# Optimization experiments

Measured on AMD Instinct MI355X. Metric: run time of the kernel, lower is better.

Reference implementation:

```python
import jax, jax.numpy as jnp
from jax import lax
import numpy as np

BATCH, SEQ, VOCAB, EMB, UNIT = 256, 512, 50000, 128, 512


def setup_inputs() -> dict:
    key = jax.random.key(0)
    ks = jax.random.split(key, 8)
    s = 0.05  # keep tanh out of saturation
    return {
        "tokens": jax.random.randint(ks[0], (BATCH, SEQ), 0, VOCAB, dtype=jnp.int32),
        "emb": jax.random.normal(ks[1], (VOCAB, EMB), jnp.float32) * s,
        "Wx0": jax.random.normal(ks[2], (EMB, UNIT), jnp.float32) * s,
        "Wh0": jax.random.normal(ks[3], (UNIT, UNIT), jnp.float32) * s,
        "b0": jnp.zeros((UNIT,), jnp.float32),
        "Wx1": jax.random.normal(ks[4], (UNIT, UNIT), jnp.float32) * s,
        "Wh1": jax.random.normal(ks[5], (UNIT, UNIT), jnp.float32) * s,
        "b1": jnp.zeros((UNIT,), jnp.float32),
        "fc_w": jax.random.normal(ks[6], (UNIT, 1), jnp.float32) * s,
        "fc_b": jnp.zeros((1,), jnp.float32),
    }


def reference(tokens, emb, Wx0, Wh0, b0, Wx1, Wh1, b1, fc_w, fc_b):
    # Embedding lookup: [B, T, E]
    x = emb[tokens]
    B = tokens.shape[0]
    U = Wh0.shape[0]

    def step(carry, xt):
        h0, h1, h2 = carry
        # SimpleRNNCell: h' = tanh(x @ Wx + h @ Wh + b); dropout inactive (training=None)
        h0n = jnp.tanh(xt @ Wx0 + h0 @ Wh0 + b0)
        # NOTE: original code reuses rnncell1 weights for both layer 1 and layer 2 (bug kept)
        h1n = jnp.tanh(h0n @ Wx1 + h1 @ Wh1 + b1)
        h2n = jnp.tanh(h1n @ Wx1 + h2 @ Wh1 + b1)
        return (h0n, h1n, h2n), None

    init = tuple(jnp.zeros((B, U), x.dtype) for _ in range(3))
    (h0, h1, h2), _ = lax.scan(step, init, jnp.swapaxes(x, 0, 1))  # scan over time [T, B, E]
    logits = h2 @ fc_w + fc_b  # [B, 1]
    return jax.nn.sigmoid(logits)
```

## Files before the change

kernel.cpp:

```cpp
#include <hip/hip_runtime.h>


#define BATCH 256
#define SEQ   512
#define EMBD  128
#define UNIT  512

typedef _Float16 half8 __attribute__((ext_vector_type(8)));
typedef _Float16 half4 __attribute__((ext_vector_type(4)));
typedef float    f32x4 __attribute__((ext_vector_type(4)));
typedef unsigned int uint4v __attribute__((ext_vector_type(4)));
typedef int      int4v __attribute__((ext_vector_type(4)));

#define FLAGS_BYTES 4096
#define HBUF_OFF    4096
#define HBUF_ELEMS  (3*8*4*32*512)
#define HBUF_BYTES  (HBUF_ELEMS*2)
#define PWX0_OFF    (HBUF_OFF + HBUF_BYTES)
#define PWH0_OFF    (PWX0_OFF + EMBD*UNIT*2)
#define PWX1_OFF    (PWH0_OFF + UNIT*UNIT*2)
#define PWH1_OFF    (PWX1_OFF + UNIT*UNIT*2)

__device__ __forceinline__ void sc_st_int(int* p, int v) {
    asm volatile("global_store_dword %0, %1, off sc0 sc1" :: "v"(p), "v"(v) : "memory");
}

__device__ __forceinline__ void sc_ld_q3(const int* p0, const int* p1, const int* p2,
                                         int4v& a, int4v& b, int4v& c) {
    asm volatile(
        "global_load_dwordx4 %0, %3, off sc0 sc1\n\t"
        "global_load_dwordx4 %1, %4, off sc0 sc1\n\t"
        "global_load_dwordx4 %2, %5, off sc0 sc1\n\t"
        "s_waitcnt vmcnt(0)"
        : "=&v"(a), "=&v"(b), "=&v"(c)
        : "v"(p0), "v"(p1), "v"(p2)
        : "memory");
}

__device__ __forceinline__ void sc_load14(
    const uint4v* a0, const uint4v* a1, const uint4v* a2,
    const uint4v* a3, const uint4v* a4, const uint4v* a5,
    const uint4v* b0, const uint4v* b1, const uint4v* b2, const uint4v* b3,
    const uint4v* b4, const uint4v* b5, const uint4v* b6, const uint4v* b7,
    uint4v& s0, uint4v& s1, uint4v& s2, uint4v& s3, uint4v& s4, uint4v& s5,
    uint4v& r0, uint4v& r1, uint4v& r2, uint4v& r3,
    uint4v& r4, uint4v& r5, uint4v& r6, uint4v& r7)
{
    asm volatile(
        "global_load_dwordx4 %0, %14, off sc0 sc1\n\t"
        "global_load_dwordx4 %1, %15, off sc0 sc1\n\t"
        "global_load_dwordx4 %2, %16, off sc0 sc1\n\t"
        "global_load_dwordx4 %3, %17, off sc0 sc1\n\t"
        "global_load_dwordx4 %4, %18, off sc0 sc1\n\t"
        "global_load_dwordx4 %5, %19, off sc0 sc1\n\t"
        "global_load_dwordx4 %6, %20, off sc0 sc1\n\t"
        "global_load_dwordx4 %7, %21, off sc0 sc1\n\t"
        "global_load_dwordx4 %8, %22, off sc0 sc1\n\t"
        "global_load_dwordx4 %9, %23, off sc0 sc1\n\t"
        "global_load_dwordx4 %10, %24, off sc0 sc1\n\t"
        "global_load_dwordx4 %11, %25, off sc0 sc1\n\t"
        "global_load_dwordx4 %12, %26, off sc0 sc1\n\t"
        "global_load_dwordx4 %13, %27, off sc0 sc1\n\t"
        "s_waitcnt vmcnt(0)"
        : "=&v"(s0), "=&v"(s1), "=&v"(s2), "=&v"(s3), "=&v"(s4), "=&v"(s5),
          "=&v"(r0), "=&v"(r1), "=&v"(r2), "=&v"(r3),
          "=&v"(r4), "=&v"(r5), "=&v"(r6), "=&v"(r7)
        : "v"(a0), "v"(a1), "v"(a2), "v"(a3), "v"(a4), "v"(a5),
          "v"(b0), "v"(b1), "v"(b2), "v"(b3), "v"(b4), "v"(b5), "v"(b6), "v"(b7)
        : "memory");
}

__device__ __forceinline__ void sc_load6(
    const uint4v* p0, const uint4v* p1, const uint4v* p2,
    const uint4v* p3, const uint4v* p4, const uint4v* p5,
    uint4v& r0, uint4v& r1, uint4v& r2, uint4v& r3, uint4v& r4, uint4v& r5)
{
    asm volatile(
        "global_load_dwordx4 %0, %6, off sc0 sc1\n\t"
        "global_load_dwordx4 %1, %7, off sc0 sc1\n\t"
        "global_load_dwordx4 %2, %8, off sc0 sc1\n\t"
        "global_load_dwordx4 %3, %9, off sc0 sc1\n\t"
        "global_load_dwordx4 %4, %10, off sc0 sc1\n\t"
        "global_load_dwordx4 %5, %11, off sc0 sc1\n\t"
        "s_waitcnt vmcnt(0)"
        : "=&v"(r0), "=&v"(r1), "=&v"(r2), "=&v"(r3), "=&v"(r4), "=&v"(r5)
        : "v"(p0), "v"(p1), "v"(p2), "v"(p3), "v"(p4), "v"(p5)
        : "memory");
}

__device__ __forceinline__ void sc_store2(uint4v* p0, uint4v v0, uint4v* p1, uint4v v1) {
    asm volatile(
        "global_store_dwordx4 %0, %2, off sc0 sc1\n\t"
        "global_store_dwordx4 %1, %3, off sc0 sc1\n\t"
        "s_waitcnt vmcnt(0)"
        :: "v"(p0), "v"(p1), "v"(v0), "v"(v1)
        : "memory");
}

__global__ void zero_ws_kernel(uint4v* __restrict__ p, int n16) {
    int i = blockIdx.x * 256 + threadIdx.x;
    uint4v z = {0u, 0u, 0u, 0u};
    if (i < n16) p[i] = z;
}

__global__ void pack_w_kernel(const float* __restrict__ src, _Float16* __restrict__ dst,
                              int K, int N) {
    int idx = blockIdx.x * 256 + threadIdx.x;
    if (idx >= K * N) return;
    int j    = idx & 7;
    int lane = (idx >> 3) & 63;
    int rest = idx >> 9;
    int KT   = K >> 5;
    int kt   = rest % KT;
    int nt   = rest / KT;
    int k = kt*32 + (lane >> 4)*8 + j;
    int n = nt*16 + (lane & 15);
    dst[idx] = (_Float16)src[k * N + n];
}

__global__ __launch_bounds__(256, 1)
void rnn_main_kernel(const int*   __restrict__ tokens,
                     const float* __restrict__ emb,
                     const float* __restrict__ b0,
                     const float* __restrict__ b1,
                     char* ws)
{
    const int bid   = blockIdx.x;
    const int layer = bid >> 5;
    const int mg    = (bid >> 2) & 7;
    const int ns    = bid & 3;
    const int tid   = threadIdx.x;
    const int wv    = tid >> 6;
    const int lane  = tid & 63;
    const int q     = lane >> 4;
    const int c16   = lane & 15;

    int* flags = (int*)ws;
    int* qOwn  = flags + (layer*8 + mg)*32;
    int* qUp   = flags + ((layer > 0 ? layer-1 : layer)*8 + mg)*32;
    int* qDn   = flags + ((layer < 2 ? layer+1 : layer)*8 + mg)*32;

    _Float16* hbuf = (_Float16*)(ws + HBUF_OFF);
    const _Float16* pWh = (const _Float16*)(ws + (layer == 0 ? PWH0_OFF : PWH1_OFF));
    const _Float16* pWx = (const _Float16*)(ws + (layer == 0 ? PWX0_OFF : PWX1_OFF));
    const float* bias = (layer == 0) ? b0 : b1;

    const int c0  = ns*128 + wv*32;
    const int nt0 = c0 >> 4;

    __shared__ _Float16 Ah [32][512];
    __shared__ _Float16 Ain[32][512];
    __shared__ _Float16 Bounce[32][128];

    {
        uint4v z = {0u,0u,0u,0u};
#pragma unroll
        for (int i = 0; i < 8; ++i) ((uint4v*)Ah)[i*256 + tid] = z;
    }

    half8 whf[16][2];
    half8 wxf[16][2];
#pragma unroll
    for (int kt = 0; kt < 16; ++kt)
#pragma unroll
        for (int n = 0; n < 2; ++n)
            whf[kt][n] = *(const half8*)&pWh[(((nt0 + n)*16 + kt)*64 + lane) * 8];
    if (layer == 0) {
#pragma unroll
        for (int kt = 0; kt < 4; ++kt)
#pragma unroll
            for (int n = 0; n < 2; ++n)
                wxf[kt][n] = *(const half8*)&pWx[(((nt0 + n)*4 + kt)*64 + lane) * 8];
    } else {
#pragma unroll
        for (int kt = 0; kt < 16; ++kt)
#pragma unroll
            for (int n = 0; n < 2; ++n)
                wxf[kt][n] = *(const half8*)&pWx[(((nt0 + n)*16 + kt)*64 + lane) * 8];
    }

    const float bv0 = bias[c0 + c16];
    const float bv1 = bias[c0 + 16 + c16];

    const int m0       = mg * 32;
    const int slotBase = (layer*8 + mg) * 4;

    const int sA = (ns == 0) ? 1 : 0;
    const int sB = (ns <= 1) ? 2 : 1;
    const int sC = (ns <= 2) ? 3 : 2;

    for (int t = 0; t < SEQ; ++t) {
        if (tid == 0) {
            for (;;) {
                int4v o, u, d;
                sc_ld_q3(qOwn, qUp, qDn, o, u, d);
                int mo = o[0] < o[1] ? o[0] : o[1];
                mo = mo < o[2] ? mo : o[2]; mo = mo < o[3] ? mo : o[3];
                int mu = u[0] < u[1] ? u[0] : u[1];
                mu = mu < u[2] ? mu : u[2]; mu = mu < u[3] ? mu : u[3];
                int md = d[0] < d[1] ? d[0] : d[1];
                md = md < d[2] ? md : d[2]; md = md < d[3] ? md : d[3];
                bool ok = (mo >= t);
                if (layer > 0)            ok = ok && (mu >= t + 1);
                if (layer < 2 && t >= 4)  ok = ok && (md >= t - 3);
                if (ok) break;
                __builtin_amdgcn_s_sleep(1);
            }
        }
        __syncthreads();

        const uint4v* tp = (const uint4v*)(hbuf + (slotBase + ((t + 3) & 3)) * 16384);
        const int j0 = 2*tid, j1 = j0 + 1;
        const int r0i = j0 >> 4, cl0 = j0 & 15;
        const int r1i = j1 >> 4, cl1 = j1 & 15;
        const int ccA0 = sA*16 + cl0, ccA1 = sA*16 + cl1;
        const int ccB0 = sB*16 + cl0, ccB1 = sB*16 + cl1;
        const int ccC0 = sC*16 + cl0, ccC1 = sC*16 + cl1;

        f32x4 acc00 = {0,0,0,0}, acc01 = {0,0,0,0}, acc10 = {0,0,0,0}, acc11 = {0,0,0,0};

        if (layer > 0) {
            const uint4v* sb = (const uint4v*)
                (hbuf + (((layer-1)*8 + mg)*4 + (t & 3)) * 16384);
            uint4v s0,s1,s2,s3,s4,s5, rr0,rr1,rr2,rr3,rr4,rr5,rr6,rr7;
            sc_load14(tp + r0i*64 + ccA0, tp + r1i*64 + ccA1,
                      tp + r0i*64 + ccB0, tp + r1i*64 + ccB1,
                      tp + r0i*64 + ccC0, tp + r1i*64 + ccC1,
                      sb +        tid, sb +  256 + tid, sb +  512 + tid, sb +  768 + tid,
                      sb + 1024 + tid, sb + 1280 + tid, sb + 1536 + tid, sb + 1792 + tid,
                      s0, s1, s2, s3, s4, s5,
                      rr0, rr1, rr2, rr3, rr4, rr5, rr6, rr7);
            *(uint4v*)&Ah[r0i][((ccA0 + r0i) & 63) * 8] = s0;
            *(uint4v*)&Ah[r1i][((ccA1 + r1i) & 63) * 8] = s1;
            *(uint4v*)&Ah[r0i][((ccB0 + r0i) & 63) * 8] = s2;
            *(uint4v*)&Ah[r1i][((ccB1 + r1i) & 63) * 8] = s3;
            *(uint4v*)&Ah[r0i][((ccC0 + r0i) & 63) * 8] = s4;
            *(uint4v*)&Ah[r1i][((ccC1 + r1i) & 63) * 8] = s5;
#pragma unroll
            for (int i = 0; i < 8; ++i) {
                uint4v v = (i==0)?rr0:(i==1)?rr1:(i==2)?rr2:(i==3)?rr3:
                           (i==4)?rr4:(i==5)?rr5:(i==6)?rr6:rr7;
                int ci = i*256 + tid;
                int r  = ci >> 6;
                int cc = ci & 63;
                *(uint4v*)&Ain[r][((cc + r) & 63) * 8] = v;
            }
            __syncthreads();

#pragma unroll
            for (int kt = 0; kt < 16; ++kt) {
                half8 a0 = *(const half8*)&Ah[c16]     [((kt*4 + q + c16)      & 63) * 8];
                half8 a1 = *(const half8*)&Ah[16 + c16][((kt*4 + q + 16 + c16) & 63) * 8];
                acc00 = __builtin_amdgcn_mfma_f32_16x16x32_f16(a0, whf[kt][0], acc00, 0, 0, 0);
                acc01 = __builtin_amdgcn_mfma_f32_16x16x32_f16(a0, whf[kt][1], acc01, 0, 0, 0);
                acc10 = __builtin_amdgcn_mfma_f32_16x16x32_f16(a1, whf[kt][0], acc10, 0, 0, 0);
                acc11 = __builtin_amdgcn_mfma_f32_16x16x32_f16(a1, whf[kt][1], acc11, 0, 0, 0);
            }
#pragma unroll
            for (int kt = 0; kt < 16; ++kt) {
                half8 a0 = *(const half8*)&Ain[c16]     [((kt*4 + q + c16)      & 63) * 8];
                half8 a1 = *(const half8*)&Ain[16 + c16][((kt*4 + q + 16 + c16) & 63) * 8];
                acc00 = __builtin_amdgcn_mfma_f32_16x16x32_f16(a0, wxf[kt][0], acc00, 0, 0, 0);
                acc01 = __builtin_amdgcn_mfma_f32_16x16x32_f16(a0, wxf[kt][1], acc01, 0, 0, 0);
                acc10 = __builtin_amdgcn_mfma_f32_16x16x32_f16(a1, wxf[kt][0], acc10, 0, 0, 0);
                acc11 = __builtin_amdgcn_mfma_f32_16x16x32_f16(a1, wxf[kt][1], acc11, 0, 0, 0);
            }
        } else {
            uint4v s0, s1, s2, s3, s4, s5;
            sc_load6(tp + r0i*64 + ccA0, tp + r1i*64 + ccA1,
                     tp + r0i*64 + ccB0, tp + r1i*64 + ccB1,
                     tp + r0i*64 + ccC0, tp + r1i*64 + ccC1,
                     s0, s1, s2, s3, s4, s5);
            *(uint4v*)&Ah[r0i][((ccA0 + r0i) & 63) * 8] = s0;
            *(uint4v*)&Ah[r1i][((ccA1 + r1i) & 63) * 8] = s1;
            *(uint4v*)&Ah[r0i][((ccB0 + r0i) & 63) * 8] = s2;
            *(uint4v*)&Ah[r1i][((ccB1 + r1i) & 63) * 8] = s3;
            *(uint4v*)&Ah[r0i][((ccC0 + r0i) & 63) * 8] = s4;
            *(uint4v*)&Ah[r1i][((ccC1 + r1i) & 63) * 8] = s5;
#pragma unroll
            for (int i = 0; i < 4; ++i) {
                int idx = i*256 + tid;
                int r   = idx >> 5;
                int qq  = idx & 31;
                int tok = tokens[(m0 + r)*SEQ + t];
                float4 f = *((const float4*)(emb + (long)tok * EMBD) + qq);
                half4 h = { (_Float16)f.x, (_Float16)f.y, (_Float16)f.z, (_Float16)f.w };
                *(half4*)&Ain[r][((((qq >> 1) + r) & 63) * 8) + (qq & 1) * 4] = h;
            }
            __syncthreads();

#pragma unroll
            for (int kt = 0; kt < 16; ++kt) {
                half8 a0 = *(const half8*)&Ah[c16]     [((kt*4 + q + c16)      & 63) * 8];
                half8 a1 = *(const half8*)&Ah[16 + c16][((kt*4 + q + 16 + c16) & 63) * 8];
                acc00 = __builtin_amdgcn_mfma_f32_16x16x32_f16(a0, whf[kt][0], acc00, 0, 0, 0);
                acc01 = __builtin_amdgcn_mfma_f32_16x16x32_f16(a0, whf[kt][1], acc01, 0, 0, 0);
                acc10 = __builtin_amdgcn_mfma_f32_16x16x32_f16(a1, whf[kt][0], acc10, 0, 0, 0);
                acc11 = __builtin_amdgcn_mfma_f32_16x16x32_f16(a1, whf[kt][1], acc11, 0, 0, 0);
            }
#pragma unroll
            for (int kt = 0; kt < 4; ++kt) {
                half8 a0 = *(const half8*)&Ain[c16]     [((kt*4 + q + c16)      & 63) * 8];
                half8 a1 = *(const half8*)&Ain[16 + c16][((kt*4 + q + 16 + c16) & 63) * 8];
                acc00 = __builtin_amdgcn_mfma_f32_16x16x32_f16(a0, wxf[kt][0], acc00, 0, 0, 0);
                acc01 = __builtin_amdgcn_mfma_f32_16x16x32_f16(a0, wxf[kt][1], acc01, 0, 0, 0);
                acc10 = __builtin_amdgcn_mfma_f32_16x16x32_f16(a1, wxf[kt][0], acc10, 0, 0, 0);
                acc11 = __builtin_amdgcn_mfma_f32_16x16x32_f16(a1, wxf[kt][1], acc11, 0, 0, 0);
            }
        }

        _Float16 hv[16];
#pragma unroll
        for (int r = 0; r < 4; ++r) {
            int row0 = q*4 + r, row1 = 16 + row0;
            float z, e; _Float16 v;
            z = acc00[r] + bv0; e = __expf(2.0f*z); v = (_Float16)(1.0f - 2.0f/(e + 1.0f));
            hv[r*4+0] = v; Bounce[row0][wv*32 + c16]      = v;
            z = acc01[r] + bv1; e = __expf(2.0f*z); v = (_Float16)(1.0f - 2.0f/(e + 1.0f));
            hv[r*4+1] = v; Bounce[row0][wv*32 + 16 + c16] = v;
            z = acc10[r] + bv0; e = __expf(2.0f*z); v = (_Float16)(1.0f - 2.0f/(e + 1.0f));
            hv[r*4+2] = v; Bounce[row1][wv*32 + c16]      = v;
            z = acc11[r] + bv1; e = __expf(2.0f*z); v = (_Float16)(1.0f - 2.0f/(e + 1.0f));
            hv[r*4+3] = v; Bounce[row1][wv*32 + 16 + c16] = v;
        }
        __syncthreads();

        {
            int g0 = c0 + c16, g1 = c0 + 16 + c16;
#pragma unroll
            for (int r = 0; r < 4; ++r) {
                int row0 = q*4 + r, row1 = 16 + row0;
                Ah[row0][(((g0 >> 3) + row0) & 63)*8 + (g0 & 7)] = hv[r*4+0];
                Ah[row0][(((g1 >> 3) + row0) & 63)*8 + (g1 & 7)] = hv[r*4+1];
                Ah[row1][(((g0 >> 3) + row1) & 63)*8 + (g0 & 7)] = hv[r*4+2];
                Ah[row1][(((g1 >> 3) + row1) & 63)*8 + (g1 & 7)] = hv[r*4+3];
            }
            _Float16* tc = hbuf + (slotBase + (t & 3)) * 16384;
            uint4v v0 = ((const uint4v*)Bounce)[j0];
            uint4v v1 = ((const uint4v*)Bounce)[j1];
            uint4v* d0 = (uint4v*)(tc + (j0 >> 4)*512 + ns*128) + (j0 & 15);
            uint4v* d1 = (uint4v*)(tc + (j1 >> 4)*512 + ns*128) + (j1 & 15);
            sc_store2(d0, v0, d1, v1);
        }
        __syncthreads();
        if (tid == 0) sc_st_int(qOwn + ns, t + 1);
    }
}

__global__ void fc_kernel(const char* __restrict__ ws,
                          const float* __restrict__ fc_w,
                          const float* __restrict__ fc_b,
                          float* __restrict__ out)
{
    int row  = blockIdx.x;
    int lane = threadIdx.x;
    int m = row >> 5, lr = row & 31;
    const _Float16* h2 = (const _Float16*)(ws + HBUF_OFF)
                         + (((2*8 + m)*4 + 3) * 16384)
                         + lr * UNIT;
    half8 hv = *(const half8*)&h2[lane * 8];
    const float* w = fc_w + lane * 8;
    float s = 0.0f;
#pragma unroll
    for (int j = 0; j < 8; ++j) s += (float)hv[j] * w[j];
#pragma unroll
    for (int off = 32; off > 0; off >>= 1) s += __shfl_down(s, off);
    if (lane == 0) {
        float logit = s + fc_b[0];
        out[row] = 1.0f / (1.0f + __expf(-logit));
    }
}

extern "C" void kernel_launch(void* const* d_in, const int* in_sizes, int n_in,
                              void* d_out, int out_size, void* d_ws, size_t ws_size,
                              hipStream_t stream)
{
    const int*   tokens = (const int*)  d_in[0];
    const float* emb    = (const float*)d_in[1];
    const float* Wx0    = (const float*)d_in[2];
    const float* Wh0    = (const float*)d_in[3];
    const float* b0     = (const float*)d_in[4];
    const float* Wx1    = (const float*)d_in[5];
    const float* Wh1    = (const float*)d_in[6];
    const float* b1     = (const float*)d_in[7];
    const float* fcw    = (const float*)d_in[8];
    const float* fcb    = (const float*)d_in[9];
    char*  ws  = (char*)d_ws;
    float* out = (float*)d_out;

    int n16 = (FLAGS_BYTES + HBUF_BYTES) / 16;
    zero_ws_kernel<<<(n16 + 255)/256, 256, 0, stream>>>((uint4v*)ws, n16);

    pack_w_kernel<<<(EMBD*UNIT + 255)/256, 256, 0, stream>>>(Wx0, (_Float16*)(ws + PWX0_OFF), EMBD, UNIT);
    pack_w_kernel<<<(UNIT*UNIT + 255)/256, 256, 0, stream>>>(Wh0, (_Float16*)(ws + PWH0_OFF), UNIT, UNIT);
    pack_w_kernel<<<(UNIT*UNIT + 255)/256, 256, 0, stream>>>(Wx1, (_Float16*)(ws + PWX1_OFF), UNIT, UNIT);
    pack_w_kernel<<<(UNIT*UNIT + 255)/256, 256, 0, stream>>>(Wh1, (_Float16*)(ws + PWH1_OFF), UNIT, UNIT);

    rnn_main_kernel<<<96, 256, 0, stream>>>(tokens, emb, b0, b1, ws);

    fc_kernel<<<256, 64, 0, stream>>>((const char*)ws, fcw, fcb, out);
}
```

Baseline: 2.636 ms.

## Remap blocks so each batch group shares an XCD and use XCD-scope coherence

```diff
diff --git a/kernel.cpp b/kernel.cpp
--- a/kernel.cpp
+++ b/kernel.cpp
@@ -44,57 +44,104 @@
     const uint4v* b4, const uint4v* b5, const uint4v* b6, const uint4v* b7,
     uint4v& s0, uint4v& s1, uint4v& s2, uint4v& s3, uint4v& s4, uint4v& s5,
     uint4v& r0, uint4v& r1, uint4v& r2, uint4v& r3,
-    uint4v& r4, uint4v& r5, uint4v& r6, uint4v& r7)
+    uint4v& r4, uint4v& r5, uint4v& r6, uint4v& r7, bool fast)
 {
-    asm volatile(
-        "global_load_dwordx4 %0, %14, off sc0 sc1\n\t"
-        "global_load_dwordx4 %1, %15, off sc0 sc1\n\t"
-        "global_load_dwordx4 %2, %16, off sc0 sc1\n\t"
-        "global_load_dwordx4 %3, %17, off sc0 sc1\n\t"
-        "global_load_dwordx4 %4, %18, off sc0 sc1\n\t"
-        "global_load_dwordx4 %5, %19, off sc0 sc1\n\t"
-        "global_load_dwordx4 %6, %20, off sc0 sc1\n\t"
-        "global_load_dwordx4 %7, %21, off sc0 sc1\n\t"
-        "global_load_dwordx4 %8, %22, off sc0 sc1\n\t"
-        "global_load_dwordx4 %9, %23, off sc0 sc1\n\t"
-        "global_load_dwordx4 %10, %24, off sc0 sc1\n\t"
-        "global_load_dwordx4 %11, %25, off sc0 sc1\n\t"
-        "global_load_dwordx4 %12, %26, off sc0 sc1\n\t"
-        "global_load_dwordx4 %13, %27, off sc0 sc1\n\t"
-        "s_waitcnt vmcnt(0)"
-        : "=&v"(s0), "=&v"(s1), "=&v"(s2), "=&v"(s3), "=&v"(s4), "=&v"(s5),
-          "=&v"(r0), "=&v"(r1), "=&v"(r2), "=&v"(r3),
-          "=&v"(r4), "=&v"(r5), "=&v"(r6), "=&v"(r7)
-        : "v"(a0), "v"(a1), "v"(a2), "v"(a3), "v"(a4), "v"(a5),
-          "v"(b0), "v"(b1), "v"(b2), "v"(b3), "v"(b4), "v"(b5), "v"(b6), "v"(b7)
-        : "memory");
+    if (fast)
+        asm volatile(
+            "global_load_dwordx4 %0, %14, off sc0\n\t"
+            "global_load_dwordx4 %1, %15, off sc0\n\t"
+            "global_load_dwordx4 %2, %16, off sc0\n\t"
+            "global_load_dwordx4 %3, %17, off sc0\n\t"
+            "global_load_dwordx4 %4, %18, off sc0\n\t"
+            "global_load_dwordx4 %5, %19, off sc0\n\t"
+            "global_load_dwordx4 %6, %20, off sc0\n\t"
+            "global_load_dwordx4 %7, %21, off sc0\n\t"
+            "global_load_dwordx4 %8, %22, off sc0\n\t"
+            "global_load_dwordx4 %9, %23, off sc0\n\t"
+            "global_load_dwordx4 %10, %24, off sc0\n\t"
+            "global_load_dwordx4 %11, %25, off sc0\n\t"
+            "global_load_dwordx4 %12, %26, off sc0\n\t"
+            "global_load_dwordx4 %13, %27, off sc0\n\t"
+            "s_waitcnt vmcnt(0)"
+            : "=&v"(s0), "=&v"(s1), "=&v"(s2), "=&v"(s3), "=&v"(s4), "=&v"(s5),
+              "=&v"(r0), "=&v"(r1), "=&v"(r2), "=&v"(r3),
+              "=&v"(r4), "=&v"(r5), "=&v"(r6), "=&v"(r7)
+            : "v"(a0), "v"(a1), "v"(a2), "v"(a3), "v"(a4), "v"(a5),
+              "v"(b0), "v"(b1), "v"(b2), "v"(b3), "v"(b4), "v"(b5), "v"(b6), "v"(b7)
+            : "memory");
+    else
+        asm volatile(
+            "global_load_dwordx4 %0, %14, off sc0 sc1\n\t"
+            "global_load_dwordx4 %1, %15, off sc0 sc1\n\t"
+            "global_load_dwordx4 %2, %16, off sc0 sc1\n\t"
+            "global_load_dwordx4 %3, %17, off sc0 sc1\n\t"
+            "global_load_dwordx4 %4, %18, off sc0 sc1\n\t"
+            "global_load_dwordx4 %5, %19, off sc0 sc1\n\t"
+            "global_load_dwordx4 %6, %20, off sc0 sc1\n\t"
+            "global_load_dwordx4 %7, %21, off sc0 sc1\n\t"
+            "global_load_dwordx4 %8, %22, off sc0 sc1\n\t"
+            "global_load_dwordx4 %9, %23, off sc0 sc1\n\t"
+            "global_load_dwordx4 %10, %24, off sc0 sc1\n\t"
+            "global_load_dwordx4 %11, %25, off sc0 sc1\n\t"
+            "global_load_dwordx4 %12, %26, off sc0 sc1\n\t"
+            "global_load_dwordx4 %13, %27, off sc0 sc1\n\t"
+            "s_waitcnt vmcnt(0)"
+            : "=&v"(s0), "=&v"(s1), "=&v"(s2), "=&v"(s3), "=&v"(s4), "=&v"(s5),
+              "=&v"(r0), "=&v"(r1), "=&v"(r2), "=&v"(r3),
+              "=&v"(r4), "=&v"(r5), "=&v"(r6), "=&v"(r7)
+            : "v"(a0), "v"(a1), "v"(a2), "v"(a3), "v"(a4), "v"(a5),
+              "v"(b0), "v"(b1), "v"(b2), "v"(b3), "v"(b4), "v"(b5), "v"(b6), "v"(b7)
+            : "memory");
 }
 
 __device__ __forceinline__ void sc_load6(
     const uint4v* p0, const uint4v* p1, const uint4v* p2,
     const uint4v* p3, const uint4v* p4, const uint4v* p5,
-    uint4v& r0, uint4v& r1, uint4v& r2, uint4v& r3, uint4v& r4, uint4v& r5)
+    uint4v& r0, uint4v& r1, uint4v& r2, uint4v& r3, uint4v& r4, uint4v& r5,
+    bool fast)
 {
-    asm volatile(
-        "global_load_dwordx4 %0, %6, off sc0 sc1\n\t"
-        "global_load_dwordx4 %1, %7, off sc0 sc1\n\t"
-        "global_load_dwordx4 %2, %8, off sc0 sc1\n\t"
-        "global_load_dwordx4 %3, %9, off sc0 sc1\n\t"
-        "global_load_dwordx4 %4, %10, off sc0 sc1\n\t"
-        "global_load_dwordx4 %5, %11, off sc0 sc1\n\t"
-        "s_waitcnt vmcnt(0)"
-        : "=&v"(r0), "=&v"(r1), "=&v"(r2), "=&v"(r3), "=&v"(r4), "=&v"(r5)
-        : "v"(p0), "v"(p1), "v"(p2), "v"(p3), "v"(p4), "v"(p5)
-        : "memory");
-}
-
-__device__ __forceinline__ void sc_store2(uint4v* p0, uint4v v0, uint4v* p1, uint4v v1) {
-    asm volatile(
-        "global_store_dwordx4 %0, %2, off sc0 sc1\n\t"
-        "global_store_dwordx4 %1, %3, off sc0 sc1\n\t"
-        "s_waitcnt vmcnt(0)"
-        :: "v"(p0), "v"(p1), "v"(v0), "v"(v1)
-        : "memory");
+    if (fast)
+        asm volatile(
+            "global_load_dwordx4 %0, %6, off sc0\n\t"
+            "global_load_dwordx4 %1, %7, off sc0\n\t"
+            "global_load_dwordx4 %2, %8, off sc0\n\t"
+            "global_load_dwordx4 %3, %9, off sc0\n\t"
+            "global_load_dwordx4 %4, %10, off sc0\n\t"
+            "global_load_dwordx4 %5, %11, off sc0\n\t"
+            "s_waitcnt vmcnt(0)"
+            : "=&v"(r0), "=&v"(r1), "=&v"(r2), "=&v"(r3), "=&v"(r4), "=&v"(r5)
+            : "v"(p0), "v"(p1), "v"(p2), "v"(p3), "v"(p4), "v"(p5)
+            : "memory");
+    else
+        asm volatile(
+            "global_load_dwordx4 %0, %6, off sc0 sc1\n\t"
+            "global_load_dwordx4 %1, %7, off sc0 sc1\n\t"
+            "global_load_dwordx4 %2, %8, off sc0 sc1\n\t"
+            "global_load_dwordx4 %3, %9, off sc0 sc1\n\t"
+            "global_load_dwordx4 %4, %10, off sc0 sc1\n\t"
+            "global_load_dwordx4 %5, %11, off sc0 sc1\n\t"
+            "s_waitcnt vmcnt(0)"
+            : "=&v"(r0), "=&v"(r1), "=&v"(r2), "=&v"(r3), "=&v"(r4), "=&v"(r5)
+            : "v"(p0), "v"(p1), "v"(p2), "v"(p3), "v"(p4), "v"(p5)
+            : "memory");
+}
+
+__device__ __forceinline__ void sc_store2(uint4v* p0, uint4v v0, uint4v* p1, uint4v v1,
+                                          bool fast) {
+    if (fast)
+        asm volatile(
+            "global_store_dwordx4 %0, %2, off sc0\n\t"
+            "global_store_dwordx4 %1, %3, off sc0\n\t"
+            "s_waitcnt vmcnt(0)"
+            :: "v"(p0), "v"(p1), "v"(v0), "v"(v1)
+            : "memory");
+    else
+        asm volatile(
+            "global_store_dwordx4 %0, %2, off sc0 sc1\n\t"
+            "global_store_dwordx4 %1, %3, off sc0 sc1\n\t"
+            "s_waitcnt vmcnt(0)"
+            :: "v"(p0), "v"(p1), "v"(v0), "v"(v1)
+            : "memory");
 }
 
 __global__ void zero_ws_kernel(uint4v* __restrict__ p, int n16) {
@@ -126,9 +173,10 @@
                      char* ws)
 {
     const int bid   = blockIdx.x;
-    const int layer = bid >> 5;
-    const int mg    = (bid >> 2) & 7;
-    const int ns    = bid & 3;
+    const int mg    = bid & 7;
+    const int inner = bid >> 3;
+    const int layer = inner >> 2;
+    const int ns    = inner & 3;
     const int tid   = threadIdx.x;
     const int wv    = tid >> 6;
     const int lane  = tid & 63;
@@ -139,6 +187,7 @@
     int* qOwn  = flags + (layer*8 + mg)*32;
     int* qUp   = flags + ((layer > 0 ? layer-1 : layer)*8 + mg)*32;
     int* qDn   = flags + ((layer < 2 ? layer+1 : layer)*8 + mg)*32;
+    int* xslots = flags + 768;
 
     _Float16* hbuf = (_Float16*)(ws + HBUF_OFF);
     const _Float16* pWh = (const _Float16*)(ws + (layer == 0 ? PWH0_OFF : PWH1_OFF));
@@ -151,6 +200,25 @@
     __shared__ _Float16 Ah [32][512];
     __shared__ _Float16 Ain[32][512];
     __shared__ _Float16 Bounce[32][128];
+    __shared__ int fastsh;
+
+    if (tid == 0) {
+        unsigned xcc;
+        asm volatile("s_getreg_b32 %0, hwreg(HW_REG_XCC_ID)" : "=s"(xcc));
+        sc_st_int(xslots + bid, (int)(xcc & 0xFu) + 1);
+        int id0 = 0; bool same = true;
+        for (int i = 0; i < 12; ++i) {
+            int v;
+            for (;;) {
+                asm volatile("global_load_dword %0, %1, off sc0 sc1\n\ts_waitcnt vmcnt(0)"
+                             : "=v"(v) : "v"(xslots + (mg + 8*i)) : "memory");
+                if (v != 0) break;
+                __builtin_amdgcn_s_sleep(1);
+            }
+            if (i == 0) id0 = v; else same = same && (v == id0);
+        }
+        fastsh = same ? 1 : 0;
+    }
 
     {
         uint4v z = {0u,0u,0u,0u};
@@ -188,6 +256,9 @@
     const int sA = (ns == 0) ? 1 : 0;
     const int sB = (ns <= 1) ? 2 : 1;
     const int sC = (ns <= 2) ? 3 : 2;
+
+    __syncthreads();
+    const bool fastp = (fastsh != 0);
 
     for (int t = 0; t < SEQ; ++t) {
         if (tid == 0) {
@@ -229,7 +300,7 @@
                       sb +        tid, sb +  256 + tid, sb +  512 + tid, sb +  768 + tid,
                       sb + 1024 + tid, sb + 1280 + tid, sb + 1536 + tid, sb + 1792 + tid,
                       s0, s1, s2, s3, s4, s5,
-                      rr0, rr1, rr2, rr3, rr4, rr5, rr6, rr7);
+                      rr0, rr1, rr2, rr3, rr4, rr5, rr6, rr7, fastp);
             *(uint4v*)&Ah[r0i][((ccA0 + r0i) & 63) * 8] = s0;
             *(uint4v*)&Ah[r1i][((ccA1 + r1i) & 63) * 8] = s1;
             *(uint4v*)&Ah[r0i][((ccB0 + r0i) & 63) * 8] = s2;
@@ -270,7 +341,7 @@
             sc_load6(tp + r0i*64 + ccA0, tp + r1i*64 + ccA1,
                      tp + r0i*64 + ccB0, tp + r1i*64 + ccB1,
                      tp + r0i*64 + ccC0, tp + r1i*64 + ccC1,
-                     s0, s1, s2, s3, s4, s5);
+                     s0, s1, s2, s3, s4, s5, fastp);
             *(uint4v*)&Ah[r0i][((ccA0 + r0i) & 63) * 8] = s0;
             *(uint4v*)&Ah[r1i][((ccA1 + r1i) & 63) * 8] = s1;
             *(uint4v*)&Ah[r0i][((ccB0 + r0i) & 63) * 8] = s2;
@@ -340,7 +411,7 @@
             uint4v v1 = ((const uint4v*)Bounce)[j1];
             uint4v* d0 = (uint4v*)(tc + (j0 >> 4)*512 + ns*128) + (j0 & 15);
             uint4v* d1 = (uint4v*)(tc + (j1 >> 4)*512 + ns*128) + (j1 & 15);
-            sc_store2(d0, v0, d1, v1);
+            sc_store2(d0, v0, d1, v1, fastp);
         }
         __syncthreads();
         if (tid == 0) sc_st_int(qOwn + ns, t + 1);
```

Result: faster. 2.572 ms (-2.4%).
